# Kernel optimization log

Measured on AMD Instinct MI355X. Metric: run time of the kernel, lower is better.

The kernel has to match this reference:

```python
import jax, jax.numpy as jnp
import numpy as np

B, N, C_IN, C_INTER = 32, 2048, 512, 512


def setup_inputs() -> dict:
    key = jax.random.key(0)
    ks = jax.random.split(key, 10)
    s_in = 1.0 / np.sqrt(C_IN)
    s_int = 1.0 / np.sqrt(C_INTER)
    return {
        "query": jax.random.normal(ks[0], (B, N, C_IN), jnp.float32),
        "key": jax.random.normal(ks[1], (B, N, C_IN), jnp.float32),
        "Wq": jax.random.normal(ks[2], (C_IN, C_INTER), jnp.float32) * s_in,
        "bq": jnp.zeros((C_INTER,), jnp.float32),
        "Wk": jax.random.normal(ks[3], (C_IN, C_INTER), jnp.float32) * s_in,
        "bk": jnp.zeros((C_INTER,), jnp.float32),
        "Wv": jax.random.normal(ks[4], (C_IN, C_INTER), jnp.float32) * s_in,
        "bv": jnp.zeros((C_INTER,), jnp.float32),
        "Wo": jax.random.normal(ks[5], (C_INTER, C_INTER), jnp.float32) * s_int,
        "bo": jnp.zeros((C_INTER,), jnp.float32),
    }


def reference(query, key, Wq, bq, Wk, bk, Wv, bv, Wo, bo):
    value = key  # value defaults to key in original forward
    q = jnp.einsum("bnc,cd->bnd", query, Wq) + bq   # [B,N,D]
    k = jnp.einsum("bnc,cd->bnd", key, Wk) + bk
    v = jnp.einsum("bnc,cd->bnd", value, Wv) + bv
    d = q.shape[-1]
    # non-standard scaling: divide by d (not sqrt(d))
    scores = jnp.einsum("bqd,bkd->bqk", q, k) / d    # [B,N,N]
    attn = jax.nn.softmax(scores, axis=-1)
    n_kv = attn.shape[-1]
    # second non-standard scaling: divide by number of keys
    out = jnp.einsum("bqk,bkd->bqd", attn, v) / n_kv
    return jnp.einsum("bnd,de->bne", out, Wo) + bo
```

## Files before the change

### kernel.cpp

```cpp
#include <hip/hip_runtime.h>
#include <stdint.h>

typedef unsigned short u16;
typedef __attribute__((ext_vector_type(8))) short bf16x8;
typedef __attribute__((ext_vector_type(4))) float f32x4;

__device__ __forceinline__ float bf2f(u16 u) {
  union { unsigned int i; float f; } v; v.i = ((unsigned int)u) << 16; return v.f;
}
__device__ __forceinline__ u16 f2bf(float f) {
  union { float f; unsigned int i; } v; v.f = f;
  unsigned int x = v.i;
  return (u16)((x + 0x7fffu + ((x >> 16) & 1u)) >> 16);
}

__device__ __forceinline__ void async16(const void* g, void* l) {
  __builtin_amdgcn_global_load_lds(
      (const __attribute__((address_space(1))) void*)g,
      (__attribute__((address_space(3))) void*)l, 16, 0, 0);
}

__global__ __launch_bounds__(256) void cast_f32_to_bf16(
    const float* __restrict__ x, u16* __restrict__ y, long n) {
  long i = ((long)blockIdx.x * blockDim.x + threadIdx.x) * 8;
  long stride = (long)gridDim.x * blockDim.x * 8;
  for (long j = i; j < n; j += stride) {
    float4 a = ((const float4*)(x + j))[0];
    float4 b = ((const float4*)(x + j))[1];
    unsigned int p0 = (unsigned)f2bf(a.x) | ((unsigned)f2bf(a.y) << 16);
    unsigned int p1 = (unsigned)f2bf(a.z) | ((unsigned)f2bf(a.w) << 16);
    unsigned int p2 = (unsigned)f2bf(b.x) | ((unsigned)f2bf(b.y) << 16);
    unsigned int p3 = (unsigned)f2bf(b.z) | ((unsigned)f2bf(b.w) << 16);
    *(uint4*)(y + j) = make_uint4(p0, p1, p2, p3);
  }
}

__global__ __launch_bounds__(256) void castWT(
    const float* __restrict__ Wq, const float* __restrict__ Wk,
    const float* __restrict__ Wv, const float* __restrict__ Wo,
    u16* __restrict__ WT) {
  int idx = blockIdx.x * 256 + threadIdx.x;
  int m = blockIdx.y;
  const float* src = (m == 0) ? Wq : (m == 1) ? Wk : (m == 2) ? Wv : Wo;
  int nn = idx >> 9;
  int cc = idx & 511;
  WT[(long)m * 262144 + idx] = f2bf(src[cc * 512 + nn]);
}

#define WAITVM8 asm volatile("s_waitcnt vmcnt(8)" ::: "memory")
#define WAITVM4 asm volatile("s_waitcnt vmcnt(4)" ::: "memory")
#define WAITVM0 asm volatile("s_waitcnt vmcnt(0)" ::: "memory")

#define TILE_BODY(T, DOSTAGE, VMWAIT)                                          \
  do {                                                                         \
    char* rb = lds + ((T) & 3) * 32768;                                        \
    bf16x8 bfr[4], afr[4];                                                     \
    _Pragma("unroll") for (int ni = 0; ni < 4; ++ni)                           \
        bfr[ni] = *(const bf16x8*)(rb + boff + ni * 1024);                     \
    _Pragma("unroll") for (int mi = 0; mi < 4; ++mi)                           \
        afr[mi] = *(const bf16x8*)(rb + aoff + mi * 1024);                     \
    if (DOSTAGE) {                                                             \
      char* sb = lds + (((T) + 3) & 3) * 32768 + ldsW;                         \
      async16(pa, sb);                                                         \
      async16(pa + 128 * (long)K, sb + 8192);                                  \
    }                                                                          \
    __builtin_amdgcn_s_barrier();                                              \
    __builtin_amdgcn_s_setprio(1);                                             \
    _Pragma("unroll") for (int mi = 0; mi < 4; ++mi)                           \
        _Pragma("unroll") for (int ni = 0; ni < 4; ++ni)                       \
            acc[mi][ni] = __builtin_amdgcn_mfma_f32_16x16x32_bf16(             \
                afr[mi], bfr[ni], acc[mi][ni], 0, 0, 0);                       \
    __builtin_amdgcn_s_setprio(0);                                             \
    __builtin_amdgcn_s_barrier();                                              \
    _Pragma("unroll") for (int mi = 0; mi < 4; ++mi)                           \
        afr[mi] = *(const bf16x8*)(rb + aoff + (mi + 4) * 1024);               \
    if (DOSTAGE) {                                                             \
      char* sb = lds + (((T) + 3) & 3) * 32768 + 16384 + ldsW;                 \
      async16(pb, sb);                                                         \
      async16(pb + 128 * (long)K, sb + 8192);                                  \
      pa += 32; pb += 32;                                                      \
    }                                                                          \
    __builtin_amdgcn_s_barrier();                                              \
    __builtin_amdgcn_s_setprio(1);                                             \
    _Pragma("unroll") for (int mi = 0; mi < 4; ++mi)                           \
        _Pragma("unroll") for (int ni = 0; ni < 4; ++ni)                       \
            acc[mi + 4][ni] = __builtin_amdgcn_mfma_f32_16x16x32_bf16(         \
                afr[mi], bfr[ni], acc[mi + 4][ni], 0, 0, 0);                   \
    __builtin_amdgcn_s_setprio(0);                                             \
    VMWAIT;                                                                    \
    __builtin_amdgcn_s_barrier();                                              \
  } while (0)

template <int MODE>
__global__ __launch_bounds__(512, 2) void gemm256(
    const u16* __restrict__ A, const u16* __restrict__ B,
    const float* __restrict__ bias, void* __restrict__ Cout,
    int N, int K, long sA, long sB, long sC, float scale) {
  __shared__ __align__(16) char lds[4 * 32768];
  const int t = threadIdx.x;
  const int lane = t & 63;
  const int w = t >> 6;
  const int wm = w >> 2;
  const int wn = w & 3;
  const long z = blockIdx.z;
  const long m0 = (long)blockIdx.x * 256;
  const int n0 = blockIdx.y * 256;
  const int nt = K >> 5;

  const int srow = w * 16 + (lane >> 2);
  const int koff = 8 * ((lane & 3) ^ ((lane >> 3) & 3));
  const int ldsW = w * 1024;
  const u16* pa = A + z * sA + (m0 + srow) * (long)K + koff;
  const u16* pb = B + z * sB + ((long)(n0 + srow)) * K + koff;

  const int frow = lane & 15;
  const int kb = (lane >> 4) * 16;
  const int sw = ((frow >> 1) & 3) << 4;
  const int aoff = (wm * 128 + frow) * 64 + (kb ^ sw);
  const int boff = 16384 + (wn * 64 + frow) * 64 + (kb ^ sw);

  f32x4 acc[8][4] = {};

#pragma unroll
  for (int pt = 0; pt < 3; ++pt) {
    char* sb = lds + pt * 32768 + ldsW;
    async16(pa, sb);
    async16(pa + 128 * (long)K, sb + 8192);
    async16(pb, sb + 16384);
    async16(pb + 128 * (long)K, sb + 24576);
    pa += 32;
    pb += 32;
  }
  WAITVM8;
  __builtin_amdgcn_s_barrier();

  for (int tt = 0; tt < nt - 3; ++tt) TILE_BODY(tt, true, WAITVM8);
  TILE_BODY(nt - 3, false, WAITVM4);
  TILE_BODY(nt - 2, false, WAITVM0);
  TILE_BODY(nt - 1, false, (void)0);

  const int er = (lane >> 4) * 4;
  const int ec = lane & 15;
  if (MODE == 0) {
    u16* Ep = (u16*)lds;
    u16* Cp = (u16*)Cout + z * sC;
    float bv[4];
#pragma unroll
    for (int ni = 0; ni < 4; ++ni)
      bv[ni] = bias ? bias[n0 + wn * 64 + ni * 16 + ec] : 0.0f;
#pragma unroll
    for (int p = 0; p < 2; ++p) {
      __syncthreads();
#pragma unroll
      for (int m2 = 0; m2 < 4; ++m2) {
#pragma unroll
        for (int ni = 0; ni < 4; ++ni) {
#pragma unroll
          for (int i = 0; i < 4; ++i) {
            float val = acc[p * 4 + m2][ni][i] * scale + bv[ni];
            Ep[(wm * 64 + m2 * 16 + er + i) * 264 + wn * 64 + ni * 16 + ec] =
                f2bf(val);
          }
        }
      }
      __syncthreads();
#pragma unroll
      for (int s = 0; s < 8; ++s) {
        int R = w * 2 + (lane >> 5) + s * 16;
        int j = lane & 31;
        uint4 d = *(const uint4*)(Ep + R * 264 + j * 8);
        long gm = m0 + (R >> 6) * 128 + p * 64 + (R & 63);
        *(uint4*)(Cp + gm * (long)N + n0 + j * 8) = d;
      }
    }
  } else {
#pragma unroll
    for (int mi = 0; mi < 8; ++mi) {
#pragma unroll
      for (int ni = 0; ni < 4; ++ni) {
#pragma unroll
        for (int i = 0; i < 4; ++i) {
          long gm = m0 + wm * 128 + mi * 16 + er + i;
          int gc = n0 + wn * 64 + ni * 16 + ec;
          float val = acc[mi][ni][i] * scale;
          if (bias) val += bias[gc];
          if (MODE == 1) {
            long b = gm >> 11, rr = gm & 2047;
            ((u16*)Cout)[b * ((long)N * 2048) + (long)gc * 2048 + rr] = f2bf(val);
          } else {
            ((float*)Cout + z * sC)[gm * (long)N + gc] = val;
          }
        }
      }
    }
  }
}

__global__ __launch_bounds__(256) void softmax_rows(u16* __restrict__ S, float inv) {
  long row = blockIdx.x;
  u16* p = S + row * 2048;
  int t = threadIdx.x;
  int lane = t & 63, wv = t >> 6;

  uint4 raw = ((const uint4*)p)[t];
  unsigned int wd[4] = {raw.x, raw.y, raw.z, raw.w};
  float v[8];
#pragma unroll
  for (int j = 0; j < 4; ++j) {
    v[2 * j]     = bf2f((u16)(wd[j] & 0xffffu));
    v[2 * j + 1] = bf2f((u16)(wd[j] >> 16));
  }
  float mx = v[0];
#pragma unroll
  for (int j = 1; j < 8; ++j) mx = fmaxf(mx, v[j]);
  for (int off = 32; off; off >>= 1) mx = fmaxf(mx, __shfl_xor(mx, off));
  __shared__ float rmax[4], rsum[4];
  if (lane == 0) rmax[wv] = mx;
  __syncthreads();
  mx = fmaxf(fmaxf(rmax[0], rmax[1]), fmaxf(rmax[2], rmax[3]));

  float e[8], s = 0.f;
#pragma unroll
  for (int j = 0; j < 8; ++j) { e[j] = __expf(v[j] - mx); s += e[j]; }
  for (int off = 32; off; off >>= 1) s += __shfl_xor(s, off);
  if (lane == 0) rsum[wv] = s;
  __syncthreads();
  s = rsum[0] + rsum[1] + rsum[2] + rsum[3];

  float r = inv / s;
  unsigned int o[4];
#pragma unroll
  for (int j = 0; j < 4; ++j)
    o[j] = (unsigned)f2bf(e[2 * j] * r) | ((unsigned)f2bf(e[2 * j + 1] * r) << 16);
  ((uint4*)p)[t] = make_uint4(o[0], o[1], o[2], o[3]);
}

extern "C" void kernel_launch(void* const* d_in, const int* in_sizes, int n_in,
                              void* d_out, int out_size, void* d_ws, size_t ws_size,
                              hipStream_t stream) {
  const float* query = (const float*)d_in[0];
  const float* key_  = (const float*)d_in[1];
  const float* Wq = (const float*)d_in[2];
  const float* bq = (const float*)d_in[3];
  const float* Wk = (const float*)d_in[4];
  const float* bk = (const float*)d_in[5];
  const float* Wv = (const float*)d_in[6];
  const float* bv = (const float*)d_in[7];
  const float* Wo = (const float*)d_in[8];
  const float* bo = (const float*)d_in[9];
  float* out = (float*)d_out;

  const long tokE = 65536L * 512;
  const long bstride = 2048L * 512;

  char* ws = (char*)d_ws;
  u16* Qb = (u16*)(ws);
  u16* Kb = (u16*)(ws + 67108864L);
  u16* vT = (u16*)(ws + 134217728L);
  u16* WT = (u16*)(ws + 201326592L);
  char* Sbase = ws + 203423744L;
  u16* attn = Qb;

  u16* qb = (u16*)d_out;
  u16* kb = (u16*)((char*)d_out + 67108864L);

  long s_avail = (long)ws_size - 203423744L;
  int g = (int)(s_avail / 8388608L);
  if (g < 1) g = 1;
  if (g > 32) g = 32;

  cast_f32_to_bf16<<<16384, 256, 0, stream>>>(query, Qb, tokE);
  cast_f32_to_bf16<<<16384, 256, 0, stream>>>(key_, Kb, tokE);
  castWT<<<dim3(1024, 4, 1), 256, 0, stream>>>(Wq, Wk, Wv, Wo, WT);

  dim3 gproj(256, 2, 1);
  gemm256<0><<<gproj, 512, 0, stream>>>(Qb, WT,           bq, qb, 512, 512, 0, 0, 0, 1.0f);
  gemm256<0><<<gproj, 512, 0, stream>>>(Kb, WT + 262144L, bk, kb, 512, 512, 0, 0, 0, 1.0f);
  gemm256<1><<<gproj, 512, 0, stream>>>(Kb, WT + 524288L, bv, vT, 512, 512, 0, 0, 0, 1.0f);

  for (int b0 = 0; b0 < 32; b0 += g) {
    int bc = (32 - b0 < g) ? (32 - b0) : g;
    u16* Sg = (u16*)Sbase;
    dim3 gs(8, 8, bc);
    gemm256<0><<<gs, 512, 0, stream>>>(qb + (long)b0 * bstride, kb + (long)b0 * bstride,
                                       nullptr, Sg, 2048, 512,
                                       bstride, bstride, 2048L * 2048, 1.0f / 512.0f);
    softmax_rows<<<bc * 2048, 256, 0, stream>>>(Sg, 1.0f / 2048.0f);
    dim3 gpv(8, 2, bc);
    gemm256<0><<<gpv, 512, 0, stream>>>(Sg, vT + (long)b0 * bstride, nullptr,
                                        attn + (long)b0 * bstride, 512, 2048,
                                        2048L * 2048, bstride, bstride, 1.0f);
  }

  gemm256<2><<<dim3(256, 2, 1), 512, 0, stream>>>(attn, WT + 786432L, bo, out,
                                                  512, 512, 0, 0, 0, 1.0f);
}
```

Baseline: 803.4 us.

## Software-pipeline LDS fragment reads with double-buffered B registers in GEMM loop

Replaces the tile macro with two half-phases. Each phase prefetches the next A/B fragments from LDS through inline ds_read_b128 asm while the current MFMAs run, using explicit lgkmcnt waits and sched barriers. B fragments ping-pong between two register sets. The vmcnt waits are also split per half-tile. The goal is to hide LDS read latency behind MFMA work, at the cost of more registers and fragile hand-written wait counts. The tail sequence assumes an odd count of steady-state tiles, which holds for the shapes used here.

```diff
diff --git a/kernel.cpp b/kernel.cpp
--- a/kernel.cpp
+++ b/kernel.cpp
@@ -47,48 +47,65 @@
   WT[(long)m * 262144 + idx] = f2bf(src[cc * 512 + nn]);
 }
 
-#define WAITVM8 asm volatile("s_waitcnt vmcnt(8)" ::: "memory")
-#define WAITVM4 asm volatile("s_waitcnt vmcnt(4)" ::: "memory")
-#define WAITVM0 asm volatile("s_waitcnt vmcnt(0)" ::: "memory")
-
-#define TILE_BODY(T, DOSTAGE, VMWAIT)                                          \
-  do {                                                                         \
-    char* rb = lds + ((T) & 3) * 32768;                                        \
-    bf16x8 bfr[4], afr[4];                                                     \
-    _Pragma("unroll") for (int ni = 0; ni < 4; ++ni)                           \
-        bfr[ni] = *(const bf16x8*)(rb + boff + ni * 1024);                     \
-    _Pragma("unroll") for (int mi = 0; mi < 4; ++mi)                           \
-        afr[mi] = *(const bf16x8*)(rb + aoff + mi * 1024);                     \
-    if (DOSTAGE) {                                                             \
-      char* sb = lds + (((T) + 3) & 3) * 32768 + ldsW;                         \
-      async16(pa, sb);                                                         \
-      async16(pa + 128 * (long)K, sb + 8192);                                  \
-    }                                                                          \
-    __builtin_amdgcn_s_barrier();                                              \
-    __builtin_amdgcn_s_setprio(1);                                             \
-    _Pragma("unroll") for (int mi = 0; mi < 4; ++mi)                           \
-        _Pragma("unroll") for (int ni = 0; ni < 4; ++ni)                       \
-            acc[mi][ni] = __builtin_amdgcn_mfma_f32_16x16x32_bf16(             \
-                afr[mi], bfr[ni], acc[mi][ni], 0, 0, 0);                       \
-    __builtin_amdgcn_s_setprio(0);                                             \
-    __builtin_amdgcn_s_barrier();                                              \
-    _Pragma("unroll") for (int mi = 0; mi < 4; ++mi)                           \
-        afr[mi] = *(const bf16x8*)(rb + aoff + (mi + 4) * 1024);               \
-    if (DOSTAGE) {                                                             \
-      char* sb = lds + (((T) + 3) & 3) * 32768 + 16384 + ldsW;                 \
-      async16(pb, sb);                                                         \
-      async16(pb + 128 * (long)K, sb + 8192);                                  \
-      pa += 32; pb += 32;                                                      \
-    }                                                                          \
-    __builtin_amdgcn_s_barrier();                                              \
-    __builtin_amdgcn_s_setprio(1);                                             \
-    _Pragma("unroll") for (int mi = 0; mi < 4; ++mi)                           \
-        _Pragma("unroll") for (int ni = 0; ni < 4; ++ni)                       \
-            acc[mi + 4][ni] = __builtin_amdgcn_mfma_f32_16x16x32_bf16(         \
-                afr[mi], bfr[ni], acc[mi + 4][ni], 0, 0, 0);                   \
-    __builtin_amdgcn_s_setprio(0);                                             \
-    VMWAIT;                                                                    \
-    __builtin_amdgcn_s_barrier();                                              \
+
+#define DSR4(d, adr)                                                   \
+  asm volatile("ds_read_b128 %0, %4 offset:0\n\t"                     \
+               "ds_read_b128 %1, %4 offset:1024\n\t"                   \
+               "ds_read_b128 %2, %4 offset:2048\n\t"                   \
+               "ds_read_b128 %3, %4 offset:3072"                       \
+               : "=&v"(d[0]), "=&v"(d[1]), "=&v"(d[2]), "=&v"(d[3])    \
+               : "v"(adr))
+
+#define LGKM(n)                                      \
+  asm volatile("s_waitcnt lgkmcnt(" #n ")");         \
+  __builtin_amdgcn_sched_barrier(0)
+#define VMC(n) asm volatile("s_waitcnt vmcnt(" #n ")" ::: "memory")
+#define BAR() __builtin_amdgcn_s_barrier()
+
+#define MFMA16(mh, Aset, Bset)                                               \
+  __builtin_amdgcn_s_setprio(1);                                             \
+  _Pragma("unroll") for (int mi = 0; mi < 4; ++mi)                           \
+  _Pragma("unroll") for (int ni = 0; ni < 4; ++ni)                           \
+      acc[(mh)*4 + mi][ni] = __builtin_amdgcn_mfma_f32_16x16x32_bf16(        \
+          Aset[mi], Bset[ni], acc[(mh)*4 + mi][ni], 0, 0, 0);                \
+  __builtin_amdgcn_s_setprio(0)
+
+#define PH0(T, Bcur, DOSTAGE, VMSTMT)                                  \
+  do {                                                                 \
+    if (DOSTAGE) {                                                     \
+      char* sb = lds + (((T) + 3) & 3) * 32768 + ldsW;                 \
+      async16(pa, sb);                                                 \
+      async16(pa + 128 * (long)K, sb + 8192);                          \
+      pa += 32;                                                        \
+    }                                                                  \
+    VMSTMT;                                                            \
+    BAR();                                                             \
+    { unsigned adr = ldsb + ((T)&3) * 32768 + aoff1r; DSR4(A1, adr); } \
+    LGKM(4);                                                           \
+    MFMA16(0, A0, Bcur);                                               \
+    BAR();                                                             \
+  } while (0)
+
+#define PH1(T, Bcur, Bnext, DOSTAGE, VMSTMT, DOREAD)                     \
+  do {                                                                   \
+    if (DOSTAGE) {                                                       \
+      char* sb = lds + (((T) + 3) & 3) * 32768 + 16384 + ldsW;           \
+      async16(pb, sb);                                                   \
+      async16(pb + 128 * (long)K, sb + 8192);                            \
+      pb += 32;                                                          \
+    }                                                                    \
+    VMSTMT;                                                              \
+    BAR();                                                               \
+    if (DOREAD) {                                                        \
+      unsigned s1 = ldsb + (((T) + 1) & 3) * 32768;                      \
+      DSR4(A0, s1 + aoff0r);                                             \
+      DSR4(Bnext, s1 + boffr);                                           \
+      LGKM(8);                                                           \
+    } else {                                                             \
+      LGKM(0);                                                           \
+    }                                                                    \
+    MFMA16(1, A1, Bcur);                                                 \
+    BAR();                                                               \
   } while (0)
 
 template <int MODE>
@@ -113,12 +130,16 @@
   const u16* pa = A + z * sA + (m0 + srow) * (long)K + koff;
   const u16* pb = B + z * sB + ((long)(n0 + srow)) * K + koff;
 
-  const int frow = lane & 15;
+  const int fr = lane & 15;
   const int kb = (lane >> 4) * 16;
-  const int sw = ((frow >> 1) & 3) << 4;
-  const int aoff = (wm * 128 + frow) * 64 + (kb ^ sw);
-  const int boff = 16384 + (wn * 64 + frow) * 64 + (kb ^ sw);
-
+  const int sw = ((fr >> 1) & 3) << 4;
+  const unsigned ldsb =
+      (unsigned)(uintptr_t)(__attribute__((address_space(3))) char*)lds;
+  const unsigned aoff0r = (unsigned)((wm * 128 + fr) * 64 + (kb ^ sw));
+  const unsigned aoff1r = aoff0r + 4096;
+  const unsigned boffr = (unsigned)(16384 + (wn * 64 + fr) * 64 + (kb ^ sw));
+
+  bf16x8 A0[4], A1[4], B0[4], B1[4];
   f32x4 acc[8][4] = {};
 
 #pragma unroll
@@ -131,13 +152,29 @@
     pa += 32;
     pb += 32;
   }
-  WAITVM8;
-  __builtin_amdgcn_s_barrier();
-
-  for (int tt = 0; tt < nt - 3; ++tt) TILE_BODY(tt, true, WAITVM8);
-  TILE_BODY(nt - 3, false, WAITVM4);
-  TILE_BODY(nt - 2, false, WAITVM0);
-  TILE_BODY(nt - 1, false, (void)0);
+  VMC(8);
+  BAR();
+  DSR4(A0, ldsb + aoff0r);
+  DSR4(B0, ldsb + boffr);
+
+  const int M = nt - 3;
+  int tt = 0;
+  for (; tt + 2 <= M; tt += 2) {
+    PH0(tt, B0, true, VMC(6));
+    PH1(tt, B0, B1, true, VMC(6), true);
+    PH0(tt + 1, B1, true, VMC(6));
+    PH1(tt + 1, B1, B0, true, VMC(6), true);
+  }
+  if (tt < M) {
+    PH0(tt, B0, true, VMC(6));
+    PH1(tt, B0, B1, true, VMC(6), true);
+  }
+  PH0(nt - 3, B1, false, VMC(4));
+  PH1(nt - 3, B1, B0, false, VMC(2), true);
+  PH0(nt - 2, B0, false, VMC(0));
+  PH1(nt - 2, B0, B1, false, (void)0, true);
+  PH0(nt - 1, B1, false, (void)0);
+  PH1(nt - 1, B1, B0, false, (void)0, false);
 
   const int er = (lane >> 4) * 4;
   const int ec = lane & 15;
```

Result: no change. 799.0 us (-0.5%).
